# Kernel tuning notes

Hardware: AMD Instinct MI355X
Metric: run time of the kernel (lower is better)

Reference implementation:

```python
import jax, jax.numpy as jnp
import numpy as np

EPS = 1e-12
MAX_TANH_ARG = 15.0
BALL_EPS = 1e-6

# ---- Poincare ball (curvature c = 1) primitives ----

def _sqnorm(x):
    return jnp.sum(x * x, axis=-1, keepdims=True)

def _norm(x):
    return jnp.sqrt(jnp.maximum(_sqnorm(x), EPS))

def _lam(x):
    # conformal factor lambda_x = 2 / (1 - ||x||^2)
    return 2.0 / jnp.maximum(1.0 - _sqnorm(x), EPS)

def mobius_add(x, y):
    x2, y2 = _sqnorm(x), _sqnorm(y)
    xy = jnp.sum(x * y, axis=-1, keepdims=True)
    num = (1.0 + 2.0 * xy + y2) * x + (1.0 - x2) * y
    den = 1.0 + 2.0 * xy + x2 * y2
    return num / jnp.maximum(den, EPS)

def exp0(v):
    n = _norm(v)
    return jnp.tanh(n) * v / n

def log0(y):
    n = _norm(y)
    return jnp.arctanh(jnp.clip(n, 0.0, 1.0 - BALL_EPS)) * y / n

def expmap(x, v):
    n = _norm(v)
    arg = jnp.clip(_lam(x) * n / 2.0, -MAX_TANH_ARG, MAX_TANH_ARG)
    second = jnp.tanh(arg) * v / n
    return mobius_add(x, second)

def logmap(x, y):
    m = mobius_add(-x, y)
    n = _norm(m)
    return (2.0 / _lam(x)) * jnp.arctanh(jnp.clip(n, 0.0, 1.0 - BALL_EPS)) * m / n

def dist(x, y):
    n = _norm(mobius_add(-x, y))
    return 2.0 * jnp.arctanh(jnp.clip(n, 0.0, 1.0 - BALL_EPS))[..., 0]

def gyr(u, v, w):
    # gyr[u,v]w = -(u (+) v) (+) (u (+) (v (+) w))
    return mobius_add(-mobius_add(u, v), mobius_add(u, mobius_add(v, w)))

def transp(x, y, v):
    # parallel transport from T_x to T_y on the Poincare ball
    return gyr(y, -x, v) * (_lam(x) / _lam(y))

def frechet_mean(x, iters=15):
    # Karcher-flow fixed-point iteration, init at exp0(mean of log0)
    mu = exp0(jnp.mean(log0(x), axis=0))
    for _ in range(iters):
        mu = expmap(mu, jnp.mean(logmap(mu, x), axis=0))
    return mu  # [d]


def setup_inputs() -> dict:
    key = jax.random.key(0)
    k1, k2 = jax.random.split(key)
    N, D = 200000, 128
    tang = 0.1 * jax.random.normal(k1, (N, D), dtype=jnp.float32)
    x = exp0(tang)  # points on the ball
    mean_param = 0.01 * jax.random.normal(k2, (D,), dtype=jnp.float32)
    var_param = jnp.ones((), dtype=jnp.float32)
    return {"x": x, "mean_param": mean_param, "var_param": var_param}


def reference(x, mean_param, var_param):
    # RiemannianBatchNorm forward (training path), Poincare ball c=1.
    on_manifold = exp0(mean_param)                 # [d]
    input_mean = frechet_mean(x)                   # [d] Frechet mean over batch
    input_var = jnp.mean(dist(x, input_mean) ** 2) # scalar Frechet variance
    # log-map points at the mean, transport tangent vecs to learned mean
    input_logm = transp(input_mean, on_manifold, logmap(input_mean, x))  # [N,d]
    input_logm = jnp.sqrt(var_param / (input_var + 1e-6)) * input_logm
    output = expmap(on_manifold, input_logm)       # [N,d]
    return output
```

## Files before the change

### kernel.cpp

```cpp
#include <hip/hip_runtime.h>
#include <math.h>

#define EPSV 1e-12f
#define BALLC (1.0f - 1e-6f)
#define MAXT 15.0f
#define NBM 512
#define NBO 512
#define BTO 512

#define MUF 0
#define PF 128
#define QF 256
#define SCF 384
#define OFFV 512
#define C_MM 0
#define C_PP 1
#define C_QQ 2
#define C_MP 3
#define C_MQ 4
#define C_PQ 5
#define C_TFM 6
#define C_LAMP 7
#define C_KS 8

typedef short bf16x8 __attribute__((ext_vector_type(8)));
typedef float f32x4 __attribute__((ext_vector_type(4)));

__device__ __forceinline__ float fast_tanh(float x) {
    float e = __expf(-2.f * x);
    return (1.f - e) / (1.f + e);
}
__device__ __forceinline__ float fast_atanh(float x) {
    return 0.5f * __logf((1.f + x) / (1.f - x));
}
__device__ __forceinline__ float qsum8(float v) {
    v += __shfl_xor(v, 1);
    v += __shfl_xor(v, 2);
    v += __shfl_xor(v, 4);
    return v;
}
__device__ __forceinline__ float wsum64(float v) {
    v += __shfl_xor(v, 1);
    v += __shfl_xor(v, 2);
    v += __shfl_xor(v, 4);
    v += __shfl_xor(v, 8);
    v += __shfl_xor(v, 16);
    v += __shfl_xor(v, 32);
    return v;
}
__device__ __forceinline__ unsigned cvt_pk_bf16(float lo, float hi) {
    unsigned r;
    asm volatile("v_cvt_pk_bf16_f32 %0, %1, %2" : "=v"(r) : "v"(lo), "v"(hi));
    return r;
}

__device__ __forceinline__ void taylor_weights(float X2, float* w) {
    float X2g = fmaxf(X2, 1e-8f);
    float r = __builtin_amdgcn_sqrtf(X2g);
    float rc = fminf(r, BALLC);
    float at0 = 0.5f * __logf((1.f + rc) * __builtin_amdgcn_rcpf(1.f - rc));
    float ir = __builtin_amdgcn_rcpf(r);
    float iX = ir * ir;
    float g0 = at0 * ir;
    float gd = (-1.f + at0 * (1.f - X2) * ir) * iX;
    float gm = ((1.f + X2) * 0.5f - at0 * (1.f - X2 * X2) * 0.5f * ir) * iX;
    float opx = 1.f + X2;
    w[0] = g0;
    w[1] = gd + 2.f * g0;
    w[2] = gm - (2.f + X2) * g0;
    w[3] = -g0 * opx;
    w[4] = -(gd * opx + 2.f * X2 * g0);
    w[5] = -gm * opx + g0 * opx * opx;
    w[6] = 4.f * at0 * at0;
    w[7] = -8.f * at0 * ir;
    w[8] = 4.f * at0 * opx * ir;
}

__global__ __launch_bounds__(1024) void k_moment(
        const float* __restrict__ x, float* __restrict__ vpartT,
        float* __restrict__ mpart, const int N, const int rpb, const int nbm) {
    __shared__ unsigned Xt[128 * 18];
    __shared__ unsigned Wt[128 * 18];
    __shared__ float rsm[8192];
    __shared__ float ssc[16][4];
    const int tid = threadIdx.x;
    const int w = tid >> 6;
    const int l = tid & 63;
    const int bid = blockIdx.x;
    const int r0 = bid * rpb;
    const int r1 = (r0 + rpb < N) ? (r0 + rpb) : N;
    const int li = l & 15;
    const int g = l >> 4;
    const int I0 = (w >> 2) * 2;
    const int J0 = (w & 3) * 2;

    float2 aV00 = make_float2(0.f, 0.f), aV0m = make_float2(0.f, 0.f);
    float2 aAv = make_float2(0.f, 0.f), aDd = make_float2(0.f, 0.f);
    float sA00 = 0.f, sA0m = 0.f, sD0 = 0.f, sDm = 0.f;
    f32x4 accD[2][2];
#pragma unroll
    for (int a = 0; a < 2; ++a)
#pragma unroll
        for (int b = 0; b < 2; ++b) accD[a][b] = (f32x4){0.f, 0.f, 0.f, 0.f};

    for (int rb = r0; rb < r1; rb += 32) {
        const int ra = rb + 2 * w;
        const int rbn = ra + 1;
        float2 xa = make_float2(0.f, 0.f), xb = make_float2(0.f, 0.f);
        if (ra < r1) xa = *(const float2*)(x + (size_t)ra * 128 + 2 * l);
        if (rbn < r1) xb = *(const float2*)(x + (size_t)rbn * 128 + 2 * l);
        float X2a = wsum64(xa.x * xa.x + xa.y * xa.y);
        float X2b = wsum64(xb.x * xb.x + xb.y * xb.y);
        float wta[9], wtb[9];
        if (ra < r1) {
            taylor_weights(X2a, wta);
        } else {
#pragma unroll
            for (int k = 0; k < 9; ++k) wta[k] = 0.f;
        }
        if (rbn < r1) {
            taylor_weights(X2b, wtb);
        } else {
#pragma unroll
            for (int k = 0; k < 9; ++k) wtb[k] = 0.f;
        }
        aV00.x += wta[0] * xa.x + wtb[0] * xb.x;
        aV00.y += wta[0] * xa.y + wtb[0] * xb.y;
        aV0m.x += wta[2] * xa.x + wtb[2] * xb.x;
        aV0m.y += wta[2] * xa.y + wtb[2] * xb.y;
        aAv.x  += wta[4] * xa.x + wtb[4] * xb.x;
        aAv.y  += wta[4] * xa.y + wtb[4] * xb.y;
        aDd.x  += wta[7] * xa.x + wtb[7] * xb.x;
        aDd.y  += wta[7] * xa.y + wtb[7] * xb.y;
        sA00 += wta[3] + wtb[3];
        sA0m += wta[5] + wtb[5];
        sD0  += wta[6] + wtb[6];
        sDm  += wta[8] + wtb[8];
        Xt[(2 * l) * 18 + w]     = cvt_pk_bf16(xa.x, xb.x);
        Xt[(2 * l + 1) * 18 + w] = cvt_pk_bf16(xa.y, xb.y);
        Wt[(2 * l) * 18 + w]     = cvt_pk_bf16(wta[1] * xa.x, wtb[1] * xb.x);
        Wt[(2 * l + 1) * 18 + w] = cvt_pk_bf16(wta[1] * xa.y, wtb[1] * xb.y);
        __syncthreads();
        union FU { uint2 d[2]; bf16x8 v; };
        bf16x8 af[2], bfr_[2];
#pragma unroll
        for (int a = 0; a < 2; ++a) {
            int i = (I0 + a) * 16 + li;
            FU fa;
            fa.d[0] = *(const uint2*)(Wt + i * 18 + 4 * g);
            fa.d[1] = *(const uint2*)(Wt + i * 18 + 4 * g + 2);
            af[a] = fa.v;
            int j = (J0 + a) * 16 + li;
            FU fb;
            fb.d[0] = *(const uint2*)(Xt + j * 18 + 4 * g);
            fb.d[1] = *(const uint2*)(Xt + j * 18 + 4 * g + 2);
            bfr_[a] = fb.v;
        }
#pragma unroll
        for (int a = 0; a < 2; ++a)
#pragma unroll
            for (int b = 0; b < 2; ++b)
                accD[a][b] = __builtin_amdgcn_mfma_f32_16x16x32_bf16(
                    af[a], bfr_[b], accD[a][b], 0, 0, 0);
        __syncthreads();
    }

#pragma unroll
    for (int a = 0; a < 2; ++a)
#pragma unroll
        for (int b = 0; b < 2; ++b)
#pragma unroll
            for (int r = 0; r < 4; ++r) {
                int row = (I0 + a) * 16 + g * 4 + r;
                int col = (J0 + b) * 16 + li;
                mpart[(size_t)bid * 16384 + (size_t)row * 128 + col] = accD[a][b][r];
            }

    rsm[(0 * 16 + w) * 128 + 2 * l] = aV00.x; rsm[(0 * 16 + w) * 128 + 2 * l + 1] = aV00.y;
    rsm[(1 * 16 + w) * 128 + 2 * l] = aV0m.x; rsm[(1 * 16 + w) * 128 + 2 * l + 1] = aV0m.y;
    rsm[(2 * 16 + w) * 128 + 2 * l] = aAv.x;  rsm[(2 * 16 + w) * 128 + 2 * l + 1] = aAv.y;
    rsm[(3 * 16 + w) * 128 + 2 * l] = aDd.x;  rsm[(3 * 16 + w) * 128 + 2 * l + 1] = aDd.y;
    if (l == 0) { ssc[w][0] = sA00; ssc[w][1] = sA0m; ssc[w][2] = sD0; ssc[w][3] = sDm; }
    __syncthreads();
    if (tid < 512) {
        int v = tid >> 7, c = tid & 127;
        float s = 0.f;
#pragma unroll
        for (int ww = 0; ww < 16; ++ww) s += rsm[(v * 16 + ww) * 128 + c];
        vpartT[(size_t)tid * nbm + bid] = s;
    }
    if (tid < 4) {
        float s = 0.f;
#pragma unroll
        for (int ww = 0; ww < 16; ++ww) s += ssc[ww][tid];
        vpartT[(size_t)(512 + tid) * nbm + bid] = s;
    }
}

__global__ __launch_bounds__(256) void k_redM(const float* __restrict__ mpart,
                                              float* __restrict__ mfin,
                                              const int nbm) {
    int e = blockIdx.x * 256 + threadIdx.x;
    float s = 0.f;
#pragma unroll 4
    for (int b = 0; b < nbm; ++b) s += mpart[(size_t)b * 16384 + e];
    mfin[e] = s;
}

__global__ __launch_bounds__(64) void k_redV(const float* __restrict__ vpartT,
                                             float* __restrict__ vfin,
                                             const int nbm) {
    int e = blockIdx.x;
    int l = threadIdx.x;
    float s = 0.f;
    for (int b = l; b < nbm; b += 64) s += vpartT[(size_t)e * nbm + b];
    s = wsum64(s);
    if (l == 0) vfin[e] = s;
}

__global__ __launch_bounds__(1024) void k_iter(
        const float* __restrict__ mpar, const float* __restrict__ vpar,
        float* __restrict__ ws, const float* __restrict__ vfin,
        const float* __restrict__ mfin, const float invN) {
    __shared__ float Msh[16384];
    __shared__ float varr[516];
    __shared__ float msum[128];
    __shared__ __align__(16) float lmu[128];
    __shared__ float lsc[2];
    const int tid = threadIdx.x;
    for (int e = tid; e < 16384; e += 1024) Msh[e] = mfin[e];
    if (tid < 516) varr[tid] = vfin[tid];
    if (tid < 128) { lmu[tid] = 0.f; msum[tid] = 0.f; }
    if (tid == 0) lsc[0] = 0.f;
    __syncthreads();

    const float* V00 = varr;
    const float* V0m = varr + 128;
    const float* Avec = varr + 256;
    const float* Dvec = varr + 384;

    for (int it = 0; it <= 15; ++it) {
        if (it > 0) {
            int i = tid >> 3, j8 = tid & 7;
            float p = 0.f;
#pragma unroll
            for (int jj = 0; jj < 16; ++jj) {
                int j = j8 + 8 * jj;
                p += Msh[i * 128 + j] * lmu[j];
            }
            p = qsum8(p);
            if (j8 == 0) msum[i] = p;
            __syncthreads();
        }
        if (tid < 64) {
            int c0 = 2 * tid, c1 = c0 + 1;
            float mm = lsc[0];
            float mu0 = lmu[c0], mu1 = lmu[c1];
            float dotA = wsum64(Avec[c0] * mu0 + Avec[c1] * mu1);
            float Sal = varr[512] + mm * varr[513] + dotA;
            float ms0 = (it > 0) ? msum[c0] : 0.f;
            float ms1 = (it > 0) ? msum[c1] : 0.f;
            float v0 = (V00[c0] + mm * V0m[c0] + ms0 + Sal * mu0) * invN;
            float v1 = (V00[c1] + mm * V0m[c1] + ms1 + Sal * mu1) * invN;
            float v2 = wsum64(v0 * v0 + v1 * v1);
            float nv = sqrtf(fmaxf(v2, EPSV));
            float lam = 2.f / fmaxf(1.f - mm, EPSV);
            float arg = fminf(lam * nv * 0.5f, MAXT);
            float tt = fast_tanh(arg);
            float sc = tt / nv;
            float sec0 = sc * v0, sec1 = sc * v1;
            float xy = wsum64(mu0 * sec0 + mu1 * sec1);
            float s2n = wsum64(sec0 * sec0 + sec1 * sec1);
            float A = 1.f + 2.f * xy + s2n;
            float B = 1.f - mm;
            float den = fmaxf(1.f + 2.f * xy + mm * s2n, EPSV);
            float idn = 1.f / den;
            float mun0 = (A * mu0 + B * sec0) * idn;
            float mun1 = (A * mu1 + B * sec1) * idn;
            float mm2 = wsum64(mun0 * mun0 + mun1 * mun1);
            lmu[c0] = mun0; lmu[c1] = mun1;
            if (tid == 0) lsc[0] = mm2;
        }
        __syncthreads();
    }

    if (tid < 64) {
        int c0 = 2 * tid, c1 = c0 + 1;
        float mm = lsc[0];
        float mu0 = lmu[c0], mu1 = lmu[c1];
        float dotD = wsum64(Dvec[c0] * mu0 + Dvec[c1] * mu1);
        float input_var = (varr[514] + mm * varr[515] + dotD) * invN;
        float mp0 = mpar[c0], mp1 = mpar[c1];
        float mpn2 = wsum64(mp0 * mp0 + mp1 * mp1);
        float pn = sqrtf(fmaxf(mpn2, EPSV));
        float th = fast_tanh(pn) / pn;
        float p0 = th * mp0, p1 = th * mp1;
        float pp = wsum64(p0 * p0 + p1 * p1);
        float pm = wsum64(p0 * mu0 + p1 * mu1);
        float A = 1.f - 2.f * pm + mm;
        float B = 1.f - pp;
        float den = fmaxf(1.f - 2.f * pm + pp * mm, EPSV);
        float q0 = (B * mu0 - A * p0) / den;
        float q1 = (B * mu1 - A * p1) / den;
        float qq = wsum64(q0 * q0 + q1 * q1);
        float mq = wsum64(mu0 * q0 + mu1 * q1);
        float pq = wsum64(p0 * q0 + p1 * q1);
        float tfm = fmaxf(1.f - mm, EPSV);
        float tfp = fmaxf(1.f - pp, EPSV);
        float lam_p = 2.f / tfp;
        float svar = sqrtf(vpar[0] / (input_var + 1e-6f));
        float ks = (tfp / tfm) * svar;
        ws[MUF + c0] = mu0; ws[MUF + c1] = mu1;
        ws[PF + c0] = p0;   ws[PF + c1] = p1;
        ws[QF + c0] = q0;   ws[QF + c1] = q1;
        if (tid == 0) {
            float* sc_ = ws + SCF;
            sc_[C_MM] = mm; sc_[C_PP] = pp; sc_[C_QQ] = qq; sc_[C_MP] = pm;
            sc_[C_MQ] = mq; sc_[C_PQ] = pq; sc_[C_TFM] = tfm;
            sc_[C_LAMP] = lam_p; sc_[C_KS] = ks;
        }
    }
}

__global__ __launch_bounds__(BTO) void k_out(const float* __restrict__ x,
                                             float* __restrict__ out,
                                             const float* __restrict__ ws,
                                             const int N, const int rpc) {
    const float* sc = ws + SCF;
    const float mm = sc[C_MM], pp = sc[C_PP], qq = sc[C_QQ];
    const float smp = sc[C_MP], smq = sc[C_MQ], spq = sc[C_PQ];
    const float tfm = sc[C_TFM], lam_p = sc[C_LAMP], ks = sc[C_KS];
    const int tid = threadIdx.x;
    const int lane = tid & 63;
    const int sub = lane & 7;
    const int grp = tid >> 3;
    const int bid = blockIdx.x;
    const float4* mu4 = (const float4*)(ws + MUF);
    const float4* p4 = (const float4*)(ws + PF);
    const float4* qv4 = (const float4*)(ws + QF);
    float4 mur[4], pr[4], qr[4];
#pragma unroll
    for (int k = 0; k < 4; ++k) {
        mur[k] = mu4[k * 8 + sub];
        pr[k] = p4[k * 8 + sub];
        qr[k] = qv4[k * 8 + sub];
    }
    const int chunk = (bid & 7) * (NBO / 8) + (bid >> 3);
    const int r0 = chunk * rpc;
    const int r1 = (r0 + rpc < N) ? (r0 + rpc) : N;
    for (int row = r0 + grp; row < r1; row += 64) {
        const float4* xr = (const float4*)(x + (size_t)row * 128);
        float4 xv[4];
#pragma unroll
        for (int k = 0; k < 4; ++k) xv[k] = xr[k * 8 + sub];
        float am = 0.f, ap = 0.f, aq = 0.f, an = 0.f;
#pragma unroll
        for (int k = 0; k < 4; ++k) {
            am += mur[k].x * xv[k].x + mur[k].y * xv[k].y + mur[k].z * xv[k].z + mur[k].w * xv[k].w;
            ap += pr[k].x * xv[k].x + pr[k].y * xv[k].y + pr[k].z * xv[k].z + pr[k].w * xv[k].w;
            aq += qr[k].x * xv[k].x + qr[k].y * xv[k].y + qr[k].z * xv[k].z + qr[k].w * xv[k].w;
            an += xv[k].x * xv[k].x + xv[k].y * xv[k].y + xv[k].z * xv[k].z + xv[k].w * xv[k].w;
        }
        float Dm = qsum8(am), Dp = qsum8(ap), Dq = qsum8(aq), X2 = qsum8(an);

        float A = 1.f - 2.f * Dm + X2;
        float B = 1.f - mm;
        float den = fmaxf(1.f - 2.f * Dm + mm * X2, EPSV);
        float iv = 1.f / den;
        float m_cm = -A * iv, m_cx = B * iv;
        float m_dm = (-A * mm + B * Dm) * iv;
        float m_dp = (-A * smp + B * Dp) * iv;
        float m_dq = (-A * smq + B * Dq) * iv;
        float m_n2 = (A * A * mm - 2.f * A * B * Dm + B * B * X2) * iv * iv;

        float n1 = sqrtf(fmaxf(m_n2, EPSV));
        float s1 = tfm * fast_atanh(fminf(n1, BALLC)) / n1;
        float t_cm = s1 * m_cm, t_cx = s1 * m_cx;
        float t_dm = s1 * m_dm, t_dp = s1 * m_dp, t_dq = s1 * m_dq;
        float t_n2 = s1 * s1 * m_n2;

        float xy = -t_dm, y2 = t_n2;
        A = 1.f + 2.f * xy + y2;
        B = 1.f - mm;
        den = fmaxf(1.f + 2.f * xy + mm * y2, EPSV);
        iv = 1.f / den;
        float w_cm = (-A + B * t_cm) * iv;
        float w_cx = B * t_cx * iv;
        float w_dp = (-A * smp + B * t_dp) * iv;
        float w_dq = (-A * smq + B * t_dq) * iv;
        float w_n2 = (A * A * mm + 2.f * A * B * xy + B * B * y2) * iv * iv;

        xy = w_dp; y2 = w_n2;
        A = 1.f + 2.f * xy + y2;
        B = 1.f - pp;
        den = fmaxf(1.f + 2.f * xy + pp * y2, EPSV);
        iv = 1.f / den;
        float w2_cm = B * w_cm * iv;
        float w2_cp = A * iv;
        float w2_cx = B * w_cx * iv;
        float w2_dp = (A * pp + B * w_dp) * iv;
        float w2_dq = (A * spq + B * w_dq) * iv;
        float w2_n2 = (A * A * pp + 2.f * A * B * xy + B * B * y2) * iv * iv;

        xy = w2_dq; y2 = w2_n2;
        A = 1.f + 2.f * xy + y2;
        B = 1.f - qq;
        den = fmaxf(1.f + 2.f * xy + qq * y2, EPSV);
        iv = 1.f / den;
        float w3_cm = B * w2_cm * iv;
        float w3_cp = B * w2_cp * iv;
        float w3_cq = A * iv;
        float w3_cx = B * w2_cx * iv;
        float w3_dp = (A * spq + B * w2_dp) * iv;
        float w3_n2 = (A * A * qq + 2.f * A * B * xy + B * B * y2) * iv * iv;

        float u_n2 = ks * ks * w3_n2;
        float nu = sqrtf(fmaxf(u_n2, EPSV));
        float arg = fminf(fmaxf(lam_p * nu * 0.5f, -MAXT), MAXT);
        float sf = fast_tanh(arg) * ks / nu;
        float s_cm = sf * w3_cm, s_cp = sf * w3_cp, s_cq = sf * w3_cq, s_cx = sf * w3_cx;
        float s_dp = sf * w3_dp;
        float s_n2 = sf * sf * w3_n2;

        xy = s_dp; y2 = s_n2;
        A = 1.f + 2.f * xy + y2;
        B = 1.f - pp;
        den = fmaxf(1.f + 2.f * xy + pp * y2, EPSV);
        iv = 1.f / den;
        float o_cm = B * s_cm * iv;
        float o_cp = (A + B * s_cp) * iv;
        float o_cq = B * s_cq * iv;
        float o_cx = B * s_cx * iv;

        float4* orow = (float4*)(out + (size_t)row * 128);
#pragma unroll
        for (int k = 0; k < 4; ++k) {
            float4 mk = mur[k], pk = pr[k], qk = qr[k], xk = xv[k];
            float4 ov;
            ov.x = o_cm * mk.x + o_cp * pk.x + o_cq * qk.x + o_cx * xk.x;
            ov.y = o_cm * mk.y + o_cp * pk.y + o_cq * qk.y + o_cx * xk.y;
            ov.z = o_cm * mk.z + o_cp * pk.z + o_cq * qk.z + o_cx * xk.z;
            ov.w = o_cm * mk.w + o_cp * pk.w + o_cq * qk.w + o_cx * xk.w;
            orow[k * 8 + sub] = ov;
        }
    }
}

extern "C" void kernel_launch(void* const* d_in, const int* in_sizes, int n_in,
                              void* d_out, int out_size, void* d_ws, size_t ws_size,
                              hipStream_t stream) {
    const float* x = (const float*)d_in[0];
    const float* mpar = (const float*)d_in[1];
    const float* vpar = (const float*)d_in[2];
    float* out = (float*)d_out;
    float* ws = (float*)d_ws;
    int N = in_sizes[0] / 128;
    float invN = 1.f / (float)N;

    long wsf = (long)(ws_size / sizeof(float));
    int nbm = NBM;
    long need = OFFV + (long)nbm * 520 + 520 + 16384 + (long)nbm * 16384;
    if (wsf < need) {
        long nb = (wsf - OFFV - 520 - 16384) / 16904;
        nbm = (nb < 8) ? 8 : (int)nb;
        if (nbm > NBM) nbm = NBM;
    }
    int rpb = (N + nbm - 1) / nbm;
    int rpo = (N + NBO - 1) / NBO;
    float* vpartT = ws + OFFV;
    float* vfin = vpartT + (long)nbm * 520;
    float* mfin = vfin + 520;
    float* mpart = mfin + 16384;

    hipLaunchKernelGGL(k_moment, dim3(nbm), dim3(1024), 0, stream,
                       x, vpartT, mpart, N, rpb, nbm);
    hipLaunchKernelGGL(k_redM, dim3(64), dim3(256), 0, stream, mpart, mfin, nbm);
    hipLaunchKernelGGL(k_redV, dim3(516), dim3(64), 0, stream, vpartT, vfin, nbm);
    hipLaunchKernelGGL(k_iter, dim3(1), dim3(1024), 0, stream,
                       mpar, vpar, ws, vfin, mfin, invN);
    hipLaunchKernelGGL(k_out, dim3(NBO), dim3(BTO), 0, stream, x, out, ws, N, rpo);
}
```

Measured before the change: 185.2 us.

## Double-buffer the moment kernel's LDS tiles and double the moment block count

```diff
diff --git a/kernel.cpp b/kernel.cpp
--- a/kernel.cpp
+++ b/kernel.cpp
@@ -4,7 +4,7 @@
 #define EPSV 1e-12f
 #define BALLC (1.0f - 1e-6f)
 #define MAXT 15.0f
-#define NBM 512
+#define NBM 1024
 #define NBO 512
 #define BTO 512
 
@@ -79,9 +79,7 @@
 __global__ __launch_bounds__(1024) void k_moment(
         const float* __restrict__ x, float* __restrict__ vpartT,
         float* __restrict__ mpart, const int N, const int rpb, const int nbm) {
-    __shared__ unsigned Xt[128 * 18];
-    __shared__ unsigned Wt[128 * 18];
-    __shared__ float rsm[8192];
+    __shared__ unsigned stash[2][2][2304];
     __shared__ float ssc[16][4];
     const int tid = threadIdx.x;
     const int w = tid >> 6;
@@ -103,67 +101,85 @@
 #pragma unroll
         for (int b = 0; b < 2; ++b) accD[a][b] = (f32x4){0.f, 0.f, 0.f, 0.f};
 
-    for (int rb = r0; rb < r1; rb += 32) {
-        const int ra = rb + 2 * w;
-        const int rbn = ra + 1;
-        float2 xa = make_float2(0.f, 0.f), xb = make_float2(0.f, 0.f);
-        if (ra < r1) xa = *(const float2*)(x + (size_t)ra * 128 + 2 * l);
-        if (rbn < r1) xb = *(const float2*)(x + (size_t)rbn * 128 + 2 * l);
-        float X2a = wsum64(xa.x * xa.x + xa.y * xa.y);
-        float X2b = wsum64(xb.x * xb.x + xb.y * xb.y);
-        float wta[9], wtb[9];
-        if (ra < r1) {
-            taylor_weights(X2a, wta);
-        } else {
-#pragma unroll
-            for (int k = 0; k < 9; ++k) wta[k] = 0.f;
-        }
-        if (rbn < r1) {
-            taylor_weights(X2b, wtb);
-        } else {
-#pragma unroll
-            for (int k = 0; k < 9; ++k) wtb[k] = 0.f;
-        }
-        aV00.x += wta[0] * xa.x + wtb[0] * xb.x;
-        aV00.y += wta[0] * xa.y + wtb[0] * xb.y;
-        aV0m.x += wta[2] * xa.x + wtb[2] * xb.x;
-        aV0m.y += wta[2] * xa.y + wtb[2] * xb.y;
-        aAv.x  += wta[4] * xa.x + wtb[4] * xb.x;
-        aAv.y  += wta[4] * xa.y + wtb[4] * xb.y;
-        aDd.x  += wta[7] * xa.x + wtb[7] * xb.x;
-        aDd.y  += wta[7] * xa.y + wtb[7] * xb.y;
-        sA00 += wta[3] + wtb[3];
-        sA0m += wta[5] + wtb[5];
-        sD0  += wta[6] + wtb[6];
-        sDm  += wta[8] + wtb[8];
-        Xt[(2 * l) * 18 + w]     = cvt_pk_bf16(xa.x, xb.x);
-        Xt[(2 * l + 1) * 18 + w] = cvt_pk_bf16(xa.y, xb.y);
-        Wt[(2 * l) * 18 + w]     = cvt_pk_bf16(wta[1] * xa.x, wtb[1] * xb.x);
-        Wt[(2 * l + 1) * 18 + w] = cvt_pk_bf16(wta[1] * xa.y, wtb[1] * xb.y);
+#define STAGE(BUF, TILE)                                                      \
+    do {                                                                      \
+        const int ra = r0 + (TILE) * 32 + 2 * w;                              \
+        const int rb2 = ra + 1;                                               \
+        float2 xa = make_float2(0.f, 0.f), xb2 = make_float2(0.f, 0.f);       \
+        if (ra < r1) xa = *(const float2*)(x + (size_t)ra * 128 + 2 * l);     \
+        if (rb2 < r1) xb2 = *(const float2*)(x + (size_t)rb2 * 128 + 2 * l);  \
+        float X2a = wsum64(xa.x * xa.x + xa.y * xa.y);                        \
+        float X2b = wsum64(xb2.x * xb2.x + xb2.y * xb2.y);                    \
+        float wta[9], wtb[9];                                                 \
+        if (ra < r1) {                                                        \
+            taylor_weights(X2a, wta);                                         \
+        } else {                                                              \
+            _Pragma("unroll") for (int k = 0; k < 9; ++k) wta[k] = 0.f;       \
+        }                                                                     \
+        if (rb2 < r1) {                                                       \
+            taylor_weights(X2b, wtb);                                         \
+        } else {                                                              \
+            _Pragma("unroll") for (int k = 0; k < 9; ++k) wtb[k] = 0.f;       \
+        }                                                                     \
+        aV00.x += wta[0] * xa.x + wtb[0] * xb2.x;                             \
+        aV00.y += wta[0] * xa.y + wtb[0] * xb2.y;                             \
+        aV0m.x += wta[2] * xa.x + wtb[2] * xb2.x;                             \
+        aV0m.y += wta[2] * xa.y + wtb[2] * xb2.y;                             \
+        aAv.x  += wta[4] * xa.x + wtb[4] * xb2.x;                             \
+        aAv.y  += wta[4] * xa.y + wtb[4] * xb2.y;                             \
+        aDd.x  += wta[7] * xa.x + wtb[7] * xb2.x;                             \
+        aDd.y  += wta[7] * xa.y + wtb[7] * xb2.y;                             \
+        sA00 += wta[3] + wtb[3];                                              \
+        sA0m += wta[5] + wtb[5];                                              \
+        sD0  += wta[6] + wtb[6];                                              \
+        sDm  += wta[8] + wtb[8];                                              \
+        unsigned* Xb = &stash[BUF][0][0];                                     \
+        unsigned* Wb = &stash[BUF][1][0];                                     \
+        Xb[(2 * l) * 18 + w]     = cvt_pk_bf16(xa.x, xb2.x);                  \
+        Xb[(2 * l + 1) * 18 + w] = cvt_pk_bf16(xa.y, xb2.y);                  \
+        Wb[(2 * l) * 18 + w]     = cvt_pk_bf16(wta[1] * xa.x, wtb[1] * xb2.x);\
+        Wb[(2 * l + 1) * 18 + w] = cvt_pk_bf16(wta[1] * xa.y, wtb[1] * xb2.y);\
+    } while (0)
+
+#define MMSTEP(BUF)                                                           \
+    do {                                                                      \
+        const unsigned* Xb = &stash[BUF][0][0];                               \
+        const unsigned* Wb = &stash[BUF][1][0];                               \
+        union FU { uint2 d[2]; bf16x8 v; };                                   \
+        bf16x8 af[2], bfr_[2];                                                \
+        _Pragma("unroll")                                                     \
+        for (int a = 0; a < 2; ++a) {                                         \
+            int i = (I0 + a) * 16 + li;                                       \
+            FU fa;                                                            \
+            fa.d[0] = *(const uint2*)(Wb + i * 18 + 4 * g);                   \
+            fa.d[1] = *(const uint2*)(Wb + i * 18 + 4 * g + 2);               \
+            af[a] = fa.v;                                                     \
+            int j = (J0 + a) * 16 + li;                                       \
+            FU fb;                                                            \
+            fb.d[0] = *(const uint2*)(Xb + j * 18 + 4 * g);                   \
+            fb.d[1] = *(const uint2*)(Xb + j * 18 + 4 * g + 2);               \
+            bfr_[a] = fb.v;                                                   \
+        }                                                                     \
+        _Pragma("unroll")                                                     \
+        for (int a = 0; a < 2; ++a)                                           \
+            _Pragma("unroll")                                                 \
+            for (int b = 0; b < 2; ++b)                                       \
+                accD[a][b] = __builtin_amdgcn_mfma_f32_16x16x32_bf16(         \
+                    af[a], bfr_[b], accD[a][b], 0, 0, 0);                     \
+    } while (0)
+
+    const int nt = (r1 > r0) ? (r1 - r0 + 31) / 32 : 0;
+    if (nt > 0) {
+        STAGE(0, 0);
         __syncthreads();
-        union FU { uint2 d[2]; bf16x8 v; };
-        bf16x8 af[2], bfr_[2];
-#pragma unroll
-        for (int a = 0; a < 2; ++a) {
-            int i = (I0 + a) * 16 + li;
-            FU fa;
-            fa.d[0] = *(const uint2*)(Wt + i * 18 + 4 * g);
-            fa.d[1] = *(const uint2*)(Wt + i * 18 + 4 * g + 2);
-            af[a] = fa.v;
-            int j = (J0 + a) * 16 + li;
-            FU fb;
-            fb.d[0] = *(const uint2*)(Xt + j * 18 + 4 * g);
-            fb.d[1] = *(const uint2*)(Xt + j * 18 + 4 * g + 2);
-            bfr_[a] = fb.v;
-        }
-#pragma unroll
-        for (int a = 0; a < 2; ++a)
-#pragma unroll
-            for (int b = 0; b < 2; ++b)
-                accD[a][b] = __builtin_amdgcn_mfma_f32_16x16x32_bf16(
-                    af[a], bfr_[b], accD[a][b], 0, 0, 0);
-        __syncthreads();
-    }
+        for (int t = 0; t < nt; ++t) {
+            if (t + 1 < nt) STAGE((t + 1) & 1, t + 1);
+            MMSTEP(t & 1);
+            __syncthreads();
+        }
+    }
+#undef STAGE
+#undef MMSTEP
 
 #pragma unroll
     for (int a = 0; a < 2; ++a)
@@ -176,6 +192,7 @@
                 mpart[(size_t)bid * 16384 + (size_t)row * 128 + col] = accD[a][b][r];
             }
 
+    float* rsm = (float*)&stash[0][0][0];
     rsm[(0 * 16 + w) * 128 + 2 * l] = aV00.x; rsm[(0 * 16 + w) * 128 + 2 * l + 1] = aV00.y;
     rsm[(1 * 16 + w) * 128 + 2 * l] = aV0m.x; rsm[(1 * 16 + w) * 128 + 2 * l + 1] = aV0m.y;
     rsm[(2 * 16 + w) * 128 + 2 * l] = aAv.x;  rsm[(2 * 16 + w) * 128 + 2 * l + 1] = aAv.y;
```

New measurement: 234.2 us. 26.4% more time.
